# Optimization experiments

Hardware: AMD Instinct MI355X
Metric: run time of the kernel (lower is better)

Reference implementation:

```python
import jax, jax.numpy as jnp
import numpy as np

NHEAD = 8
STRIP = 7  # strip_width (horizontal strips, is_vertical=False)


def setup_inputs() -> dict:
    key = jax.random.key(0)
    k0, k1, k2 = jax.random.split(key, 3)
    B, H, W, C = 2, 112, 112, 256
    x = jax.random.normal(k0, (B, H * W, C), dtype=jnp.float32)
    # torch nn.Linear weights: (out_features, in_features)
    qkv_w = jax.random.normal(k1, (3 * C, C), dtype=jnp.float32) * 0.02
    proj_w = jax.random.normal(k2, (C, C), dtype=jnp.float32) * 0.02
    proj_b = jnp.zeros((C,), dtype=jnp.float32)
    return {"x": x, "qkv_w": qkv_w, "proj_w": proj_w, "proj_b": proj_b,
            "H_feat": 112, "W_feat": 112}


def reference(x, qkv_w, proj_w, proj_b, H_feat, W_feat):
    B, N, C = x.shape
    hd = C // NHEAD
    scale = hd ** -0.5
    n_strips = H_feat // STRIP
    L = STRIP * W_feat  # tokens per horizontal strip
    # window_partition with window (STRIP, W_feat): nwW==1, so a pure reshape
    xs = x.reshape(B * n_strips, L, C)
    # qkv projection (Linear: y = x @ W^T), then split q/k/v and heads
    qkv = jnp.einsum('bnc,dc->bnd', xs, qkv_w)
    qkv = qkv.reshape(B * n_strips, L, 3, NHEAD, hd)
    q, k, v = jnp.moveaxis(qkv, 2, 0)  # each (Bw, L, H, hd)
    attn = jnp.einsum('bnhd,bmhd->bhnm', q * scale, k)
    attn = jax.nn.softmax(attn, axis=-1)
    out = jnp.einsum('bhnm,bmhd->bnhd', attn, v).reshape(B * n_strips, L, C)
    out = jnp.einsum('bnc,dc->bnd', out, proj_w) + proj_b
    # window_reverse is again a pure reshape for horizontal strips
    return out.reshape(B, N, C)
```

## Files before the change

### kernel.cpp

```cpp
#include <hip/hip_runtime.h>
#include <hip/hip_bf16.h>

#define M_ROWS 25088
#define CDIM   256
#define QKVD   768
#define LWIN   784
#define NWINH  256

typedef __attribute__((ext_vector_type(8))) short short8v;
typedef __attribute__((ext_vector_type(4))) float floatx4;

#define CEQ 0.2550660106245232f

static __device__ __forceinline__ unsigned short f2bf(float f) {
    unsigned int x = __float_as_uint(f);
    x += 0x7fffu + ((x >> 16) & 1u);
    return (unsigned short)(x >> 16);
}
static __device__ __forceinline__ unsigned int cvt_pk_bf16(float a, float b) {
    unsigned int r;
    asm("v_cvt_pk_bf16_f32 %0, %1, %2" : "=v"(r) : "v"(a), "v"(b));
    return r;
}
static __device__ __forceinline__ void gld_lds16(const unsigned short* g,
                                                 unsigned short* l) {
    __builtin_amdgcn_global_load_lds(
        (const __attribute__((address_space(1))) unsigned int*)g,
        (__attribute__((address_space(3))) unsigned int*)l, 16, 0, 0);
}

__global__ __launch_bounds__(256) void k_f2bf(
    const float* __restrict__ src, unsigned short* __restrict__ dst, int n8)
{
    const float4* s4 = (const float4*)src;
    uint4* d4 = (uint4*)dst;
    for (int i = blockIdx.x * 256 + threadIdx.x; i < n8;
         i += gridDim.x * 256) {
        float4 a = s4[2 * i], b = s4[2 * i + 1];
        uint4 o;
        o.x = cvt_pk_bf16(a.x, a.y);
        o.y = cvt_pk_bf16(a.z, a.w);
        o.z = cvt_pk_bf16(b.x, b.y);
        o.w = cvt_pk_bf16(b.z, b.w);
        d4[i] = o;
    }
}

template <typename OUT_T, bool BIAS, bool SCALEQ>
__global__ __launch_bounds__(256, 2) void k_gemm_mfma(
    const unsigned short* __restrict__ A,
    const unsigned short* __restrict__ B,
    const float* __restrict__ bias,
    OUT_T* __restrict__ Y, int N)
{
    __shared__ __attribute__((aligned(16))) unsigned short As[128 * 64];
    __shared__ __attribute__((aligned(16))) unsigned short Bs[128 * 64];
    const int t = threadIdx.x;
    const int lane = t & 63, wv = t >> 6;
    const int lq = lane & 15, g = lane >> 4;
    const int wm = wv >> 1, wn = wv & 1;
    const int R0 = blockIdx.y * 128, C0 = blockIdx.x * 128;
    const int lrow = t >> 3, lch = (t & 7) * 8;

    floatx4 acc[4][4];
#pragma unroll
    for (int i = 0; i < 4; ++i)
#pragma unroll
        for (int j = 0; j < 4; ++j) acc[i][j] = (floatx4){0.f, 0.f, 0.f, 0.f};

    for (int kc = 0; kc < 256; kc += 64) {
#pragma unroll
        for (int i = 0; i < 4; ++i) {
            gld_lds16(A + (size_t)(R0 + i * 32 + lrow) * 256 + kc + lch,
                      As + (i * 32 + wv * 8) * 64);
            gld_lds16(B + (size_t)(C0 + i * 32 + lrow) * 256 + kc + lch,
                      Bs + (i * 32 + wv * 8) * 64);
        }
        __syncthreads();
#pragma unroll
        for (int kk = 0; kk < 64; kk += 32) {
            short8v af[4], bf[4];
#pragma unroll
            for (int mi = 0; mi < 4; ++mi)
                af[mi] = *(const short8v*)(As + (wm * 64 + mi * 16 + lq) * 64 +
                                           kk + g * 8);
#pragma unroll
            for (int ni = 0; ni < 4; ++ni)
                bf[ni] = *(const short8v*)(Bs + (wn * 64 + ni * 16 + lq) * 64 +
                                           kk + g * 8);
#pragma unroll
            for (int mi = 0; mi < 4; ++mi)
#pragma unroll
                for (int ni = 0; ni < 4; ++ni)
                    acc[mi][ni] = __builtin_amdgcn_mfma_f32_16x16x32_bf16(
                        af[mi], bf[ni], acc[mi][ni], 0, 0, 0);
        }
        __syncthreads();
    }

#pragma unroll
    for (int mi = 0; mi < 4; ++mi) {
        const size_t rb = (size_t)R0 + wm * 64 + mi * 16 + g * 4;
#pragma unroll
        for (int ni = 0; ni < 4; ++ni) {
            const int col = C0 + wn * 64 + ni * 16 + lq;
            float bv = 0.f;
            if constexpr (BIAS) bv = bias[col];
#pragma unroll
            for (int r = 0; r < 4; ++r) {
                float val = acc[mi][ni][r];
                if constexpr (SCALEQ) { if (col < 256) val *= CEQ; }
                val += bv;
                if constexpr (sizeof(OUT_T) == 2)
                    Y[(rb + r) * N + col] = (OUT_T)f2bf(val);
                else
                    Y[(rb + r) * N + col] = (OUT_T)val;
            }
        }
    }
}

#define KPITCH 36
#define VPITCH 404
#define KS_SZ  (LWIN * KPITCH)
#define ATTN_LDS (KS_SZ * 2 + 32 * VPITCH * 4)

__global__ __launch_bounds__(1024, 1) void k_attn_mfma(
    const unsigned short* __restrict__ qkv,
    unsigned short* __restrict__ ao)
{
    extern __shared__ unsigned short sm[];
    unsigned short* Ks = sm;
    unsigned int*   Vt = (unsigned int*)(sm + KS_SZ);
    const int t = threadIdx.x;
    const int lane = t & 63, wave = t >> 6;
    const int lq = lane & 15, g = lane >> 4;
    const int h = blockIdx.x & 7, w = blockIdx.x >> 3;
    const size_t rowbase = (size_t)w * LWIN;
    const unsigned short* base = qkv + rowbase * QKVD;

    for (int idx = t; idx < LWIN * 4; idx += 1024) {
        const int row = idx >> 2, c = idx & 3;
        uint4 kv = *(const uint4*)(base + (size_t)row * QKVD + 256 + h * 32 + c * 8);
        *(uint4*)(Ks + row * KPITCH + c * 8) = kv;
    }
    {
        const int c = t >> 8;
        const int p0 = t & 255;
        for (int tp = p0; tp < 392; tp += 256) {
            const int u = tp >> 4, tpp = tp & 15;
            const int a = tpp >> 3, gg = (tpp >> 1) & 3, rp = tpp & 1;
            const int wrd = u * 16 + gg * 4 + a * 2 + rp;
            union { uint4 u4; unsigned short s[8]; } x0, x1;
            x0.u4 = *(const uint4*)(base + (size_t)(2 * tp) * QKVD + 512 + h * 32 + c * 8);
            x1.u4 = *(const uint4*)(base + (size_t)(2 * tp + 1) * QKVD + 512 + h * 32 + c * 8);
#pragma unroll
            for (int j = 0; j < 8; ++j)
                Vt[(c * 8 + j) * VPITCH + wrd] =
                    (unsigned int)x0.s[j] | ((unsigned int)x1.s[j] << 16);
        }
    }
    for (int idx = t; idx < 32 * 8; idx += 1024) {
        const int d = idx >> 3, q = idx & 7;
        Vt[d * VPITCH + 384 + (q >> 1) * 4 + 2 + (q & 1)] = 0;
    }
    __syncthreads();

    const int ntile = (wave == 0) ? 4 : 3;
    const int tbase = (wave == 0) ? 0 : (3 * wave + 1);

    short8v qf[4];
#pragma unroll
    for (int n = 0; n < 4; ++n)
        if (n < ntile)
            qf[n] = *(const short8v*)(base +
                    (size_t)((tbase + n) * 16 + lq) * QKVD + h * 32 + g * 8);

    floatx4 oa[4][2];
#pragma unroll
    for (int n = 0; n < 4; ++n) {
        oa[n][0] = (floatx4){0.f, 0.f, 0.f, 0.f};
        oa[n][1] = (floatx4){0.f, 0.f, 0.f, 0.f};
    }
    float lsum[4] = {0.f, 0.f, 0.f, 0.f};

    for (int u = 0; u < 25; ++u) {
        unsigned int pw[4][4];
        {
            short8v kf = *(const short8v*)(Ks + (size_t)(2 * u * 16 + lq) * KPITCH + g * 8);
#pragma unroll
            for (int n = 0; n < 4; ++n) if (n < ntile) {
                floatx4 st = __builtin_amdgcn_mfma_f32_16x16x32_bf16(
                    kf, qf[n], (floatx4){0.f, 0.f, 0.f, 0.f}, 0, 0, 0);
                float p0 = __builtin_amdgcn_exp2f(st[0]);
                float p1 = __builtin_amdgcn_exp2f(st[1]);
                float p2 = __builtin_amdgcn_exp2f(st[2]);
                float p3 = __builtin_amdgcn_exp2f(st[3]);
                lsum[n] += (p0 + p1) + (p2 + p3);
                pw[n][0] = cvt_pk_bf16(p0, p1);
                pw[n][1] = cvt_pk_bf16(p2, p3);
            }
        }
        if (u < 24) {
            short8v kf = *(const short8v*)(Ks + (size_t)((2 * u + 1) * 16 + lq) * KPITCH + g * 8);
#pragma unroll
            for (int n = 0; n < 4; ++n) if (n < ntile) {
                floatx4 st = __builtin_amdgcn_mfma_f32_16x16x32_bf16(
                    kf, qf[n], (floatx4){0.f, 0.f, 0.f, 0.f}, 0, 0, 0);
                float p0 = __builtin_amdgcn_exp2f(st[0]);
                float p1 = __builtin_amdgcn_exp2f(st[1]);
                float p2 = __builtin_amdgcn_exp2f(st[2]);
                float p3 = __builtin_amdgcn_exp2f(st[3]);
                lsum[n] += (p0 + p1) + (p2 + p3);
                pw[n][2] = cvt_pk_bf16(p0, p1);
                pw[n][3] = cvt_pk_bf16(p2, p3);
            }
        } else {
#pragma unroll
            for (int n = 0; n < 4; ++n) if (n < ntile) {
                pw[n][2] = 0u; pw[n][3] = 0u;
            }
        }
        const unsigned short* vrow0 = (const unsigned short*)Vt;
        short8v v0 = *(const short8v*)(vrow0 + (size_t)lq * (VPITCH * 2) + u * 32 + g * 8);
        short8v v1 = *(const short8v*)(vrow0 + (size_t)(lq + 16) * (VPITCH * 2) + u * 32 + g * 8);
#pragma unroll
        for (int n = 0; n < 4; ++n) if (n < ntile) {
            union { unsigned int wd[4]; short8v v; } pu;
            pu.wd[0] = pw[n][0]; pu.wd[1] = pw[n][1];
            pu.wd[2] = pw[n][2]; pu.wd[3] = pw[n][3];
            oa[n][0] = __builtin_amdgcn_mfma_f32_16x16x32_bf16(pu.v, v0, oa[n][0], 0, 0, 0);
            oa[n][1] = __builtin_amdgcn_mfma_f32_16x16x32_bf16(pu.v, v1, oa[n][1], 0, 0, 0);
        }
    }

#pragma unroll
    for (int n = 0; n < 4; ++n) if (n < ntile) {
        float l = lsum[n];
        l += __shfl_xor(l, 16);
        l += __shfl_xor(l, 32);
        float inv = 1.f / l;
        const size_t orow0 = rowbase + (size_t)(tbase + n) * 16;
#pragma unroll
        for (int r = 0; r < 4; ++r) {
            float ir = __shfl(inv, (lane & 48) | (g * 4 + r));
            size_t ob = (orow0 + g * 4 + r) * CDIM + h * 32;
            ao[ob + lq]      = f2bf(oa[n][0][r] * ir);
            ao[ob + 16 + lq] = f2bf(oa[n][1][r] * ir);
        }
    }
}

extern "C" void kernel_launch(void* const* d_in, const int* in_sizes, int n_in,
                              void* d_out, int out_size, void* d_ws, size_t ws_size,
                              hipStream_t stream) {
    const float* x      = (const float*)d_in[0];
    const float* qkv_w  = (const float*)d_in[1];
    const float* proj_w = (const float*)d_in[2];
    const float* proj_b = (const float*)d_in[3];
    float* out = (float*)d_out;

    unsigned short* qkvb = (unsigned short*)d_ws;
    unsigned short* xb   = qkvb + (size_t)M_ROWS * QKVD;
    unsigned short* aob  = xb;
    unsigned short* wqb  = xb + (size_t)M_ROWS * CDIM;
    unsigned short* wpb  = wqb + (size_t)QKVD * CDIM;

    hipFuncSetAttribute((const void*)k_attn_mfma,
                        hipFuncAttributeMaxDynamicSharedMemorySize, ATTN_LDS);

    k_f2bf<<<2048, 256, 0, stream>>>(x, xb, (M_ROWS * CDIM) / 8);
    k_f2bf<<<96, 256, 0, stream>>>(qkv_w, wqb, (QKVD * CDIM) / 8);
    k_f2bf<<<32, 256, 0, stream>>>(proj_w, wpb, (CDIM * CDIM) / 8);

    k_gemm_mfma<unsigned short, false, true>
        <<<dim3(QKVD / 128, M_ROWS / 128), 256, 0, stream>>>(
            xb, wqb, nullptr, qkvb, QKVD);

    k_attn_mfma<<<dim3(NWINH), 1024, ATTN_LDS, stream>>>(qkvb, aob);

    k_gemm_mfma<float, true, false>
        <<<dim3(CDIM / 128, M_ROWS / 128), 256, 0, stream>>>(
            aob, wpb, proj_b, out, CDIM);
}
```

Before: 88.12 us.

## Split attention query tiles across two blocks and stream K/V in two phases

The attention kernel now launches two blocks per (window, head), each taking about half of the 49 query tiles. Each wave holds at most 2 query tiles instead of 3-4. K and V are staged into LDS in two halves with a barrier between them, which cuts the LDS footprint so more blocks can be resident. The cost is that each block reloads the full K/V from global memory (doubling that traffic) and adds an extra sync per phase. The 8-blocks hint in launch_bounds may also pressure register allocation.

```diff
diff --git a/kernel.cpp b/kernel.cpp
--- a/kernel.cpp
+++ b/kernel.cpp
@@ -121,126 +121,143 @@
 }
 
 #define KPITCH 36
-#define VPITCH 404
-#define KS_SZ  (LWIN * KPITCH)
-#define ATTN_LDS (KS_SZ * 2 + 32 * VPITCH * 4)
-
-__global__ __launch_bounds__(1024, 1) void k_attn_mfma(
+#define VPITCH 212
+#define KROWS0 416
+#define KS_SH  (KROWS0 * KPITCH)
+#define ATTN_LDS (KS_SH * 2 + 32 * VPITCH * 4)
+
+__global__ __launch_bounds__(1024, 8) void k_attn_mfma(
     const unsigned short* __restrict__ qkv,
     unsigned short* __restrict__ ao)
 {
     extern __shared__ unsigned short sm[];
     unsigned short* Ks = sm;
-    unsigned int*   Vt = (unsigned int*)(sm + KS_SZ);
+    unsigned int*   Vt = (unsigned int*)(sm + KS_SH);
     const int t = threadIdx.x;
     const int lane = t & 63, wave = t >> 6;
     const int lq = lane & 15, g = lane >> 4;
-    const int h = blockIdx.x & 7, w = blockIdx.x >> 3;
+    const int wh = blockIdx.x & 255, half = blockIdx.x >> 8;
+    const int h = wh & 7, w = wh >> 3;
     const size_t rowbase = (size_t)w * LWIN;
     const unsigned short* base = qkv + rowbase * QKVD;
 
-    for (int idx = t; idx < LWIN * 4; idx += 1024) {
-        const int row = idx >> 2, c = idx & 3;
-        uint4 kv = *(const uint4*)(base + (size_t)row * QKVD + 256 + h * 32 + c * 8);
-        *(uint4*)(Ks + row * KPITCH + c * 8) = kv;
-    }
-    {
-        const int c = t >> 8;
-        const int p0 = t & 255;
-        for (int tp = p0; tp < 392; tp += 256) {
-            const int u = tp >> 4, tpp = tp & 15;
-            const int a = tpp >> 3, gg = (tpp >> 1) & 3, rp = tpp & 1;
-            const int wrd = u * 16 + gg * 4 + a * 2 + rp;
-            union { uint4 u4; unsigned short s[8]; } x0, x1;
-            x0.u4 = *(const uint4*)(base + (size_t)(2 * tp) * QKVD + 512 + h * 32 + c * 8);
-            x1.u4 = *(const uint4*)(base + (size_t)(2 * tp + 1) * QKVD + 512 + h * 32 + c * 8);
-#pragma unroll
-            for (int j = 0; j < 8; ++j)
-                Vt[(c * 8 + j) * VPITCH + wrd] =
-                    (unsigned int)x0.s[j] | ((unsigned int)x1.s[j] << 16);
-        }
-    }
-    for (int idx = t; idx < 32 * 8; idx += 1024) {
-        const int d = idx >> 3, q = idx & 7;
-        Vt[d * VPITCH + 384 + (q >> 1) * 4 + 2 + (q & 1)] = 0;
-    }
-    __syncthreads();
-
-    const int ntile = (wave == 0) ? 4 : 3;
-    const int tbase = (wave == 0) ? 0 : (3 * wave + 1);
-
-    short8v qf[4];
-#pragma unroll
-    for (int n = 0; n < 4; ++n)
+    const int tcnt = half ? 24 : 25;
+    const int toff = half ? 25 : 0;
+    const int ntile = (wave + 16 < tcnt) ? 2 : 1;
+
+    short8v qf[2];
+#pragma unroll
+    for (int n = 0; n < 2; ++n)
         if (n < ntile)
             qf[n] = *(const short8v*)(base +
-                    (size_t)((tbase + n) * 16 + lq) * QKVD + h * 32 + g * 8);
-
-    floatx4 oa[4][2];
-#pragma unroll
-    for (int n = 0; n < 4; ++n) {
+                    (size_t)((toff + wave + n * 16) * 16 + lq) * QKVD +
+                    h * 32 + g * 8);
+
+    floatx4 oa[2][2];
+#pragma unroll
+    for (int n = 0; n < 2; ++n) {
         oa[n][0] = (floatx4){0.f, 0.f, 0.f, 0.f};
         oa[n][1] = (floatx4){0.f, 0.f, 0.f, 0.f};
     }
-    float lsum[4] = {0.f, 0.f, 0.f, 0.f};
-
-    for (int u = 0; u < 25; ++u) {
-        unsigned int pw[4][4];
+    float lsum[2] = {0.f, 0.f};
+
+    for (int ph = 0; ph < 2; ++ph) {
+        const int u0 = ph ? 13 : 0, u1 = ph ? 25 : 13;
+        const int krows = ph ? 368 : 416;
+        if (ph) __syncthreads();
+
+        for (int idx = t; idx < krows * 4; idx += 1024) {
+            const int row = idx >> 2, c = idx & 3;
+            uint4 kv = *(const uint4*)(base +
+                (size_t)(KROWS0 * ph + row) * QKVD + 256 + h * 32 + c * 8);
+            *(uint4*)(Ks + row * KPITCH + c * 8) = kv;
+        }
         {
-            short8v kf = *(const short8v*)(Ks + (size_t)(2 * u * 16 + lq) * KPITCH + g * 8);
-#pragma unroll
-            for (int n = 0; n < 4; ++n) if (n < ntile) {
-                floatx4 st = __builtin_amdgcn_mfma_f32_16x16x32_bf16(
-                    kf, qf[n], (floatx4){0.f, 0.f, 0.f, 0.f}, 0, 0, 0);
-                float p0 = __builtin_amdgcn_exp2f(st[0]);
-                float p1 = __builtin_amdgcn_exp2f(st[1]);
-                float p2 = __builtin_amdgcn_exp2f(st[2]);
-                float p3 = __builtin_amdgcn_exp2f(st[3]);
-                lsum[n] += (p0 + p1) + (p2 + p3);
-                pw[n][0] = cvt_pk_bf16(p0, p1);
-                pw[n][1] = cvt_pk_bf16(p2, p3);
-            }
-        }
-        if (u < 24) {
-            short8v kf = *(const short8v*)(Ks + (size_t)((2 * u + 1) * 16 + lq) * KPITCH + g * 8);
-#pragma unroll
-            for (int n = 0; n < 4; ++n) if (n < ntile) {
-                floatx4 st = __builtin_amdgcn_mfma_f32_16x16x32_bf16(
-                    kf, qf[n], (floatx4){0.f, 0.f, 0.f, 0.f}, 0, 0, 0);
-                float p0 = __builtin_amdgcn_exp2f(st[0]);
-                float p1 = __builtin_amdgcn_exp2f(st[1]);
-                float p2 = __builtin_amdgcn_exp2f(st[2]);
-                float p3 = __builtin_amdgcn_exp2f(st[3]);
-                lsum[n] += (p0 + p1) + (p2 + p3);
-                pw[n][2] = cvt_pk_bf16(p0, p1);
-                pw[n][3] = cvt_pk_bf16(p2, p3);
-            }
-        } else {
-#pragma unroll
-            for (int n = 0; n < 4; ++n) if (n < ntile) {
-                pw[n][2] = 0u; pw[n][3] = 0u;
-            }
-        }
-        const unsigned short* vrow0 = (const unsigned short*)Vt;
-        short8v v0 = *(const short8v*)(vrow0 + (size_t)lq * (VPITCH * 2) + u * 32 + g * 8);
-        short8v v1 = *(const short8v*)(vrow0 + (size_t)(lq + 16) * (VPITCH * 2) + u * 32 + g * 8);
-#pragma unroll
-        for (int n = 0; n < 4; ++n) if (n < ntile) {
-            union { unsigned int wd[4]; short8v v; } pu;
-            pu.wd[0] = pw[n][0]; pu.wd[1] = pw[n][1];
-            pu.wd[2] = pw[n][2]; pu.wd[3] = pw[n][3];
-            oa[n][0] = __builtin_amdgcn_mfma_f32_16x16x32_bf16(pu.v, v0, oa[n][0], 0, 0, 0);
-            oa[n][1] = __builtin_amdgcn_mfma_f32_16x16x32_bf16(pu.v, v1, oa[n][1], 0, 0, 0);
-        }
-    }
-
-#pragma unroll
-    for (int n = 0; n < 4; ++n) if (n < ntile) {
+            const int c = t >> 8;
+            const int p0 = t & 255;
+            const int tp0 = ph ? 208 : 0, tpn = ph ? 184 : 208;
+            for (int tpl = p0; tpl < tpn; tpl += 256) {
+                const int tp = tp0 + tpl;
+                const int u = tp >> 4, tpp = tp & 15;
+                const int a = tpp >> 3, gg = (tpp >> 1) & 3, rp = tpp & 1;
+                const int wrd = (u - u0) * 16 + gg * 4 + a * 2 + rp;
+                union { uint4 u4; unsigned short s[8]; } x0, x1;
+                x0.u4 = *(const uint4*)(base + (size_t)(2 * tp) * QKVD + 512 + h * 32 + c * 8);
+                x1.u4 = *(const uint4*)(base + (size_t)(2 * tp + 1) * QKVD + 512 + h * 32 + c * 8);
+#pragma unroll
+                for (int j = 0; j < 8; ++j)
+                    Vt[(c * 8 + j) * VPITCH + wrd] =
+                        (unsigned int)x0.s[j] | ((unsigned int)x1.s[j] << 16);
+            }
+        }
+        if (ph) {
+            for (int idx = t; idx < 32 * 8; idx += 1024) {
+                const int d = idx >> 3, q = idx & 7;
+                Vt[d * VPITCH + 176 + (q >> 1) * 4 + 2 + (q & 1)] = 0;
+            }
+        }
+        __syncthreads();
+
+        for (int u = u0; u < u1; ++u) {
+            unsigned int pw[2][4];
+            const int lr = (u - u0) * 32 + lq;
+            {
+                short8v kf = *(const short8v*)(Ks + (size_t)lr * KPITCH + g * 8);
+#pragma unroll
+                for (int n = 0; n < 2; ++n) if (n < ntile) {
+                    floatx4 st = __builtin_amdgcn_mfma_f32_16x16x32_bf16(
+                        kf, qf[n], (floatx4){0.f, 0.f, 0.f, 0.f}, 0, 0, 0);
+                    float p0 = __builtin_amdgcn_exp2f(st[0]);
+                    float p1 = __builtin_amdgcn_exp2f(st[1]);
+                    float p2 = __builtin_amdgcn_exp2f(st[2]);
+                    float p3 = __builtin_amdgcn_exp2f(st[3]);
+                    lsum[n] += (p0 + p1) + (p2 + p3);
+                    pw[n][0] = cvt_pk_bf16(p0, p1);
+                    pw[n][1] = cvt_pk_bf16(p2, p3);
+                }
+            }
+            if (u < 24) {
+                short8v kf = *(const short8v*)(Ks + (size_t)(lr + 16) * KPITCH + g * 8);
+#pragma unroll
+                for (int n = 0; n < 2; ++n) if (n < ntile) {
+                    floatx4 st = __builtin_amdgcn_mfma_f32_16x16x32_bf16(
+                        kf, qf[n], (floatx4){0.f, 0.f, 0.f, 0.f}, 0, 0, 0);
+                    float p0 = __builtin_amdgcn_exp2f(st[0]);
+                    float p1 = __builtin_amdgcn_exp2f(st[1]);
+                    float p2 = __builtin_amdgcn_exp2f(st[2]);
+                    float p3 = __builtin_amdgcn_exp2f(st[3]);
+                    lsum[n] += (p0 + p1) + (p2 + p3);
+                    pw[n][2] = cvt_pk_bf16(p0, p1);
+                    pw[n][3] = cvt_pk_bf16(p2, p3);
+                }
+            } else {
+#pragma unroll
+                for (int n = 0; n < 2; ++n) if (n < ntile) {
+                    pw[n][2] = 0u; pw[n][3] = 0u;
+                }
+            }
+            const unsigned short* vrow0 = (const unsigned short*)Vt;
+            const int vo = (u - u0) * 32 + g * 8;
+            short8v v0 = *(const short8v*)(vrow0 + (size_t)lq * (VPITCH * 2) + vo);
+            short8v v1 = *(const short8v*)(vrow0 + (size_t)(lq + 16) * (VPITCH * 2) + vo);
+#pragma unroll
+            for (int n = 0; n < 2; ++n) if (n < ntile) {
+                union { unsigned int wd[4]; short8v v; } pu;
+                pu.wd[0] = pw[n][0]; pu.wd[1] = pw[n][1];
+                pu.wd[2] = pw[n][2]; pu.wd[3] = pw[n][3];
+                oa[n][0] = __builtin_amdgcn_mfma_f32_16x16x32_bf16(pu.v, v0, oa[n][0], 0, 0, 0);
+                oa[n][1] = __builtin_amdgcn_mfma_f32_16x16x32_bf16(pu.v, v1, oa[n][1], 0, 0, 0);
+            }
+        }
+    }
+
+#pragma unroll
+    for (int n = 0; n < 2; ++n) if (n < ntile) {
         float l = lsum[n];
         l += __shfl_xor(l, 16);
         l += __shfl_xor(l, 32);
         float inv = 1.f / l;
-        const size_t orow0 = rowbase + (size_t)(tbase + n) * 16;
+        const size_t orow0 = rowbase + (size_t)(toff + wave + n * 16) * 16;
 #pragma unroll
         for (int r = 0; r < 4; ++r) {
             float ir = __shfl(inv, (lane & 48) | (g * 4 + r));
@@ -277,7 +294,7 @@
         <<<dim3(QKVD / 128, M_ROWS / 128), 256, 0, stream>>>(
             xb, wqb, nullptr, qkvb, QKVD);
 
-    k_attn_mfma<<<dim3(NWINH), 1024, ATTN_LDS, stream>>>(qkvb, aob);
+    k_attn_mfma<<<dim3(2 * NWINH), 1024, ATTN_LDS, stream>>>(qkvb, aob);
 
     k_gemm_mfma<float, true, false>
         <<<dim3(CDIM / 128, M_ROWS / 128), 256, 0, stream>>>(
```

Measured after the change: 240.8 us. 173% more time.

## Fuse fp32-to-bf16 conversion into GEMM tile loads and raise MFMA priority in attention

Applied to the files above, without the earlier changes.

Drops the three standalone fp32-to-bf16 conversion kernels. Each GEMM now reads fp32 x and the weights directly, converts them in registers and stores bf16 tiles to LDS, which removes the extra write and re-read of the bf16 copies and two kernel launches. In exchange, the fp32 path replaces the asynchronous global-to-LDS loads with synchronous register loads, and each weight tile is converted again by every block that uses it. The attention loop also wraps its main body in s_setprio 1/0 so waves raise their scheduling priority while issuing MFMA work.

```diff
diff --git a/kernel.cpp b/kernel.cpp
--- a/kernel.cpp
+++ b/kernel.cpp
@@ -29,27 +29,10 @@
         (__attribute__((address_space(3))) unsigned int*)l, 16, 0, 0);
 }
 
-__global__ __launch_bounds__(256) void k_f2bf(
-    const float* __restrict__ src, unsigned short* __restrict__ dst, int n8)
-{
-    const float4* s4 = (const float4*)src;
-    uint4* d4 = (uint4*)dst;
-    for (int i = blockIdx.x * 256 + threadIdx.x; i < n8;
-         i += gridDim.x * 256) {
-        float4 a = s4[2 * i], b = s4[2 * i + 1];
-        uint4 o;
-        o.x = cvt_pk_bf16(a.x, a.y);
-        o.y = cvt_pk_bf16(a.z, a.w);
-        o.z = cvt_pk_bf16(b.x, b.y);
-        o.w = cvt_pk_bf16(b.z, b.w);
-        d4[i] = o;
-    }
-}
-
-template <typename OUT_T, bool BIAS, bool SCALEQ>
+template <typename OUT_T, bool BIAS, bool SCALEQ, bool A_FP32, bool B_FP32>
 __global__ __launch_bounds__(256, 2) void k_gemm_mfma(
-    const unsigned short* __restrict__ A,
-    const unsigned short* __restrict__ B,
+    const void* __restrict__ Av,
+    const void* __restrict__ Bv,
     const float* __restrict__ bias,
     OUT_T* __restrict__ Y, int N)
 {
@@ -61,6 +44,7 @@
     const int wm = wv >> 1, wn = wv & 1;
     const int R0 = blockIdx.y * 128, C0 = blockIdx.x * 128;
     const int lrow = t >> 3, lch = (t & 7) * 8;
+    const int srow = t >> 3, scol = (t & 7) * 8;
 
     floatx4 acc[4][4];
 #pragma unroll
@@ -69,12 +53,47 @@
         for (int j = 0; j < 4; ++j) acc[i][j] = (floatx4){0.f, 0.f, 0.f, 0.f};
 
     for (int kc = 0; kc < 256; kc += 64) {
-#pragma unroll
-        for (int i = 0; i < 4; ++i) {
-            gld_lds16(A + (size_t)(R0 + i * 32 + lrow) * 256 + kc + lch,
-                      As + (i * 32 + wv * 8) * 64);
-            gld_lds16(B + (size_t)(C0 + i * 32 + lrow) * 256 + kc + lch,
-                      Bs + (i * 32 + wv * 8) * 64);
+        if constexpr (A_FP32) {
+            const float* A = (const float*)Av;
+#pragma unroll
+            for (int i = 0; i < 4; ++i) {
+                const float* src = A + (size_t)(R0 + i * 32 + srow) * 256 + kc + scol;
+                float4 a0 = *(const float4*)src;
+                float4 a1 = *(const float4*)(src + 4);
+                uint4 o;
+                o.x = cvt_pk_bf16(a0.x, a0.y);
+                o.y = cvt_pk_bf16(a0.z, a0.w);
+                o.z = cvt_pk_bf16(a1.x, a1.y);
+                o.w = cvt_pk_bf16(a1.z, a1.w);
+                *(uint4*)(As + (i * 32 + srow) * 64 + scol) = o;
+            }
+        } else {
+            const unsigned short* A = (const unsigned short*)Av;
+#pragma unroll
+            for (int i = 0; i < 4; ++i)
+                gld_lds16(A + (size_t)(R0 + i * 32 + lrow) * 256 + kc + lch,
+                          As + (i * 32 + wv * 8) * 64);
+        }
+        if constexpr (B_FP32) {
+            const float* B = (const float*)Bv;
+#pragma unroll
+            for (int i = 0; i < 4; ++i) {
+                const float* src = B + (size_t)(C0 + i * 32 + srow) * 256 + kc + scol;
+                float4 b0 = *(const float4*)src;
+                float4 b1 = *(const float4*)(src + 4);
+                uint4 o;
+                o.x = cvt_pk_bf16(b0.x, b0.y);
+                o.y = cvt_pk_bf16(b0.z, b0.w);
+                o.z = cvt_pk_bf16(b1.x, b1.y);
+                o.w = cvt_pk_bf16(b1.z, b1.w);
+                *(uint4*)(Bs + (i * 32 + srow) * 64 + scol) = o;
+            }
+        } else {
+            const unsigned short* B = (const unsigned short*)Bv;
+#pragma unroll
+            for (int i = 0; i < 4; ++i)
+                gld_lds16(B + (size_t)(C0 + i * 32 + lrow) * 256 + kc + lch,
+                          Bs + (i * 32 + wv * 8) * 64);
         }
         __syncthreads();
 #pragma unroll
@@ -186,6 +205,7 @@
 
     for (int u = 0; u < 25; ++u) {
         unsigned int pw[4][4];
+        __builtin_amdgcn_s_setprio(1);
         {
             short8v kf = *(const short8v*)(Ks + (size_t)(2 * u * 16 + lq) * KPITCH + g * 8);
 #pragma unroll
@@ -232,6 +252,7 @@
             oa[n][0] = __builtin_amdgcn_mfma_f32_16x16x32_bf16(pu.v, v0, oa[n][0], 0, 0, 0);
             oa[n][1] = __builtin_amdgcn_mfma_f32_16x16x32_bf16(pu.v, v1, oa[n][1], 0, 0, 0);
         }
+        __builtin_amdgcn_s_setprio(0);
     }
 
 #pragma unroll
@@ -261,25 +282,18 @@
     float* out = (float*)d_out;
 
     unsigned short* qkvb = (unsigned short*)d_ws;
-    unsigned short* xb   = qkvb + (size_t)M_ROWS * QKVD;
-    unsigned short* aob  = xb;
-    unsigned short* wqb  = xb + (size_t)M_ROWS * CDIM;
-    unsigned short* wpb  = wqb + (size_t)QKVD * CDIM;
+    unsigned short* aob  = qkvb + (size_t)M_ROWS * QKVD;
 
     hipFuncSetAttribute((const void*)k_attn_mfma,
                         hipFuncAttributeMaxDynamicSharedMemorySize, ATTN_LDS);
 
-    k_f2bf<<<2048, 256, 0, stream>>>(x, xb, (M_ROWS * CDIM) / 8);
-    k_f2bf<<<96, 256, 0, stream>>>(qkv_w, wqb, (QKVD * CDIM) / 8);
-    k_f2bf<<<32, 256, 0, stream>>>(proj_w, wpb, (CDIM * CDIM) / 8);
-
-    k_gemm_mfma<unsigned short, false, true>
+    k_gemm_mfma<unsigned short, false, true, true, true>
         <<<dim3(QKVD / 128, M_ROWS / 128), 256, 0, stream>>>(
-            xb, wqb, nullptr, qkvb, QKVD);
+            x, qkv_w, nullptr, qkvb, QKVD);
 
     k_attn_mfma<<<dim3(NWINH), 1024, ATTN_LDS, stream>>>(qkvb, aob);
 
-    k_gemm_mfma<float, true, false>
+    k_gemm_mfma<float, true, false, false, true>
         <<<dim3(CDIM / 128, M_ROWS / 128), 256, 0, stream>>>(
-            aob, wpb, proj_b, out, CDIM);
-}
+            aob, proj_w, proj_b, out, CDIM);
+}
```

After: 107.6 us. 1.22x slower.
